# Performance work log

Measured on AMD Instinct MI355X. Metric: run time of the kernel, lower is better.

## Reference

```python
import jax, jax.numpy as jnp
import numpy as np

K = 1024   # codebook size
C = 8      # codebook channels
D = K // C # per-channel code dim = 128
BETA = 0.25
B = 8192   # batch of latent vectors, each of size C*D = K


def setup_inputs() -> dict:
    key = jax.random.key(0)
    k1, k2, k3 = jax.random.split(key, 3)
    latents = jax.random.normal(k1, (B, C * D), dtype=jnp.float32)
    # nn.Embedding(K, D) init: uniform(-1/K, 1/K)
    embedding = jax.random.uniform(k2, (K, D), dtype=jnp.float32,
                                   minval=-1.0 / K, maxval=1.0 / K)
    k = jax.random.randint(k3, (C,), 0, 8, dtype=jnp.int32)
    return {"latents": latents, "embedding": embedding, "k": k}


def reference(latents, embedding, k):
    sg = jax.lax.stop_gradient
    flat = latents.reshape(-1, D)                                  # [B*C, D]
    # squared euclidean distance to every code: [B*C, K]
    dist = (jnp.sum(flat ** 2, axis=1, keepdims=True)
            + jnp.sum(embedding ** 2, axis=1)
            - 2.0 * (flat @ embedding.T))
    order = jnp.argsort(dist, axis=1).reshape(-1, C, K)            # [B, C, K]
    # per channel c, pick the k[c]-th nearest code index
    sel = jnp.take_along_axis(order, k[None, :, None], axis=2)[..., 0]  # [B, C]
    # one-hot @ embedding == plain gather of selected rows
    quantized = embedding[sel.reshape(-1)].reshape(latents.shape)  # [B, C*D]
    commitment_loss = jnp.mean((sg(quantized) - latents) ** 2)
    embedding_loss = jnp.mean((quantized - sg(latents)) ** 2)
    vq_loss = BETA * commitment_loss + embedding_loss
    # straight-through estimator
    quantized_st = latents + sg(quantized - latents)
    return quantized_st, vq_loss
```

## Files before the change

kernel.cpp:

```cpp
#include <hip/hip_runtime.h>

#define KDIM   128
#define BM     64
#define NELEM  8388608

#define OFF_EBUF0 17408
#define OFF_ESQ   33792
#define OFF_FSQ   37888
#define OFF_SEL   38144
#define SMEM_SZ   38400

typedef __attribute__((ext_vector_type(8)))  short  short8;
typedef __attribute__((ext_vector_type(8)))  __bf16 bf16x8;
typedef __attribute__((ext_vector_type(4)))  float  f32x4;

__device__ inline ushort f2bf(float f) {
  unsigned u = __builtin_bit_cast(unsigned, f);
  u += 0x7fffu + ((u >> 16) & 1u);
  return (ushort)(u >> 16);
}
__device__ inline f32x4 mfma16(short8 a, short8 b, f32x4 c) {
  return __builtin_amdgcn_mfma_f32_16x16x32_bf16(
      __builtin_bit_cast(bf16x8, a), __builtin_bit_cast(bf16x8, b), c, 0, 0, 0);
}
__device__ inline void gload16(const void* g, void* l) {
  __builtin_amdgcn_global_load_lds(
      (const __attribute__((address_space(1))) unsigned*)g,
      (__attribute__((address_space(3))) unsigned*)l, 16, 0, 0);
}

__global__ void vq_prep(const float* __restrict__ emb, ushort* __restrict__ ebf,
                        float* __restrict__ esqm) {
  int j = blockIdx.x, d = threadIdx.x;
  float v = emb[j * KDIM + d];
  ebf[j * KDIM + (d ^ ((j & 7) << 3))] = f2bf(v);
  float s = v * v;
#pragma unroll
  for (int m = 1; m <= 32; m <<= 1) s += __shfl_xor(s, m);
  __shared__ float w[2];
  if ((threadIdx.x & 63) == 0) w[threadIdx.x >> 6] = s;
  __syncthreads();
  if (threadIdx.x == 0) esqm[j] = -0.5f * (w[0] + w[1]);
}

__global__ __launch_bounds__(256, 4) void vq_main(
    const float* __restrict__ lat, const float* __restrict__ emb,
    const int* __restrict__ ksel, const ushort* __restrict__ ebf,
    const float* __restrict__ esqm, float* __restrict__ out,
    float* __restrict__ partial) {
  __shared__ __align__(16) unsigned char smem[SMEM_SZ];
  ushort* fLds    = (ushort*)(smem);
  float*  esqmLds = (float*)(smem + OFF_ESQ);
  float*  fsqLds  = (float*)(smem + OFF_FSQ);
  int*    selLds  = (int*)(smem + OFF_SEL);

  const int tid = threadIdx.x;
  const int lane = tid & 63, wid = tid >> 6;
  const int gR0 = blockIdx.x * BM;

  {
    const char* src = (const char*)ebf + tid * 16;
    char* dst = (char*)smem + OFF_EBUF0 + tid * 16;
#pragma unroll
    for (int q = 0; q < 4; ++q) gload16(src + q * 4096, dst + q * 4096);
  }
  ((float4*)esqmLds)[tid] = ((const float4*)esqm)[tid];

#pragma unroll
  for (int it = 0; it < 8; ++it) {
    int i = tid + it * 256;
    int row = i >> 5, c4 = i & 31;
    float4 v = *(const float4*)(lat + (size_t)(gR0 + row) * KDIM + c4 * 4);
    float s = v.x * v.x + v.y * v.y + v.z * v.z + v.w * v.w;
#pragma unroll
    for (int m = 1; m <= 16; m <<= 1) s += __shfl_xor(s, m);
    if ((lane & 31) == 0) fsqLds[row] = s;
    ushort4 b; b.x = f2bf(v.x); b.y = f2bf(v.y); b.z = f2bf(v.z); b.w = f2bf(v.w);
    *(ushort4*)(&fLds[row * 136 + c4 * 4]) = b;
  }
  __syncthreads();

  const int n = lane & 15, hi = lane >> 4;
  short8 bfr[4];
  {
    const ushort* fp = &fLds[(wid * 16 + n) * 136 + hi * 8];
#pragma unroll
    for (int s = 0; s < 4; ++s) bfr[s] = *(const short8*)(fp + s * 32);
  }
  asm volatile("s_waitcnt lgkmcnt(0)" ::: "memory");

  const int nm = n & 7;
  const int pb = ((hi ^ (nm & 3)) << 4) | (((nm >> 2) & 1) << 6);
  const char* aE0 = (const char*)smem + OFF_EBUF0 + n * 256 + pb;
  const char* aO0 = (const char*)smem + OFF_EBUF0 + n * 256 + (pb ^ 64);
  const char* aE1 = (const char*)smem + 0 + n * 256 + pb;
  const char* aO1 = (const char*)smem + 0 + n * 256 + (pb ^ 64);

  int cst[4][4];
#pragma unroll
  for (int st = 0; st < 4; ++st)
#pragma unroll
    for (int r = 0; r < 4; ++r) cst[st][r] = st * 16 + hi * 4 + r;

  float top[8];
#pragma unroll
  for (int p = 0; p < 8; ++p) top[p] = __builtin_bit_cast(float, 0xFF800000u);

#pragma unroll 2
  for (int nn = 0; nn < 16; ++nn) {
    __builtin_amdgcn_s_barrier();
    if (nn < 15) {
      const char* src = (const char*)ebf + (nn + 1) * 16384 + tid * 16;
      char* dst = (char*)smem + ((nn & 1) ? OFF_EBUF0 : 0) + tid * 16;
#pragma unroll
      for (int q = 0; q < 4; ++q) gload16(src + q * 4096, dst + q * 4096);
      asm volatile("s_waitcnt vmcnt(4)" ::: "memory");
    } else {
      asm volatile("s_waitcnt vmcnt(0)" ::: "memory");
    }
    __builtin_amdgcn_s_barrier();

    const char* aEb = (nn & 1) ? aE1 : aE0;
    const char* aOb = (nn & 1) ? aO1 : aO0;

    f32x4 acc[4];
    {
      const float* eq = esqmLds + nn * 64 + hi * 4;
#pragma unroll
      for (int st = 0; st < 4; ++st) acc[st] = *(const f32x4*)(eq + st * 16);
    }

#pragma unroll
    for (int s = 0; s < 4; ++s) {
      const char* ab = (s & 1) ? aOb : aEb;
      const int so = (s >> 1) * 128;
#pragma unroll
      for (int st = 0; st < 4; ++st) {
        short8 a = *(const short8*)(ab + st * 4096 + so);
        acc[st] = mfma16(a, bfr[s], acc[st]);
      }
    }

#pragma unroll
    for (int cell = 0; cell < 2; ++cell) {
      float k[8];
#pragma unroll
      for (int st = 0; st < 2; ++st)
#pragma unroll
        for (int r = 0; r < 4; ++r) {
          unsigned bb = (__builtin_bit_cast(unsigned, acc[cell * 2 + st][r]) & 0xFFFFFC00u)
                        | (unsigned)cst[cell * 2 + st][r];
          k[st * 4 + r] = __builtin_bit_cast(float, bb);
        }
      float x = fmaxf(fmaxf(k[0], k[1]), k[2]);
      float y = fmaxf(fmaxf(k[3], k[4]), k[5]);
      float z = fmaxf(k[6], k[7]);
      float c = fmaxf(fmaxf(x, y), z);
      unsigned cb = __builtin_bit_cast(unsigned, c) | (unsigned)(nn << 6);
      float key = __builtin_bit_cast(float, cb);
#pragma unroll
      for (int p = 0; p < 8; ++p) {
        float mx = fmaxf(top[p], key);
        key = fminf(top[p], key);
        top[p] = mx;
      }
    }
  }

  float* mbuf = (float*)(smem + OFF_EBUF0);
  __syncthreads();
#pragma unroll
  for (int p = 0; p < 8; ++p) mbuf[p * 256 + tid] = top[p];
  __syncthreads();

  if (tid < 64) {
    const int b0 = (tid >> 4) * 64 + (tid & 15);
    int kk = ksel[tid & 7]; kk = kk < 0 ? 0 : (kk > 7 ? 7 : kk);
    float a0 = mbuf[b0], a1 = mbuf[b0 + 16], a2 = mbuf[b0 + 32], a3 = mbuf[b0 + 48];
    int i0 = 1, i1 = 1, i2 = 1, i3 = 1;
    float sel = a0;
    for (int s = 0; s <= kk; ++s) {
      float m01 = fmaxf(a0, a1), m23 = fmaxf(a2, a3);
      sel = fmaxf(m01, m23);
      if (sel == a0)      { a0 = mbuf[i0 * 256 + b0];      ++i0; }
      else if (sel == a1) { a1 = mbuf[i1 * 256 + b0 + 16]; ++i1; }
      else if (sel == a2) { a2 = mbuf[i2 * 256 + b0 + 32]; ++i2; }
      else                { a3 = mbuf[i3 * 256 + b0 + 48]; ++i3; }
    }
    unsigned sb = __builtin_bit_cast(unsigned, sel);
    selLds[tid] = (int)(sb & 1023u);
    float val = __builtin_bit_cast(float, sb & 0xFFFFFC00u);
    float rl = fsqLds[tid] - 2.0f * val;
#pragma unroll
    for (int m = 1; m <= 32; m <<= 1) rl += __shfl_xor(rl, m);
    if (tid == 0) partial[blockIdx.x] = rl;
  }
  __syncthreads();

#pragma unroll
  for (int it = 0; it < 8; ++it) {
    int i = tid + it * 256;
    int row = i >> 5, c4 = i & 31;
    int s2 = selLds[row];
    float4 q = *(const float4*)(emb + (size_t)s2 * KDIM + c4 * 4);
    *(float4*)(out + (size_t)(gR0 + row) * KDIM + c4 * 4) = q;
  }
}

__global__ void vq_reduce(const float* __restrict__ p, float* __restrict__ loss) {
  int t = threadIdx.x;
  double s = (double)p[t] + (double)p[t + 256] + (double)p[t + 512] + (double)p[t + 768];
#pragma unroll
  for (int m = 1; m <= 32; m <<= 1) s += __shfl_xor(s, m);
  __shared__ double w[4];
  if ((t & 63) == 0) w[t >> 6] = s;
  __syncthreads();
  if (t == 0) loss[0] = (float)((w[0] + w[1] + w[2] + w[3]) * (1.25 / 8388608.0));
}

extern "C" void kernel_launch(void* const* d_in, const int* in_sizes, int n_in,
                              void* d_out, int out_size, void* d_ws, size_t ws_size,
                              hipStream_t stream) {
  const float* lat = (const float*)d_in[0];
  const float* emb = (const float*)d_in[1];
  const int* ksel = (const int*)d_in[2];
  float* out = (float*)d_out;

  ushort* ebf = (ushort*)d_ws;
  float* esqm = (float*)((char*)d_ws + 262144);
  float* partial = (float*)((char*)d_ws + 266240);

  vq_prep<<<1024, 128, 0, stream>>>(emb, ebf, esqm);
  vq_main<<<1024, 256, 0, stream>>>(lat, emb, ksel, ebf, esqm, out, partial);
  vq_reduce<<<1, 256, 0, stream>>>(partial, out + NELEM);
}
```

Baseline: 44.49 us.

## Keep latent tiles in registers and stream codebook fragments directly from global

The main kernel no longer stages the bf16 codebook through double-buffered LDS with global-to-LDS loads. Instead each wave holds all 64 row fragments of its latent tile in registers and owns a quarter of the codebook (256 codes), loading A fragments straight from global/L2 with register double-buffering. Per-row top-8 lists are kept per wave-slice and merged across 16 sorted lists in a final 16-way selection, and the launch-bounds occupancy hint drops to 2 blocks. This removes LDS traffic and barriers in the inner loop, but raises register pressure and relies on L2 bandwidth for repeated codebook reads across all blocks.

```diff
diff --git a/kernel.cpp b/kernel.cpp
--- a/kernel.cpp
+++ b/kernel.cpp
@@ -3,12 +3,12 @@
 #define KDIM   128
 #define BM     64
 #define NELEM  8388608
-
-#define OFF_EBUF0 17408
-#define OFF_ESQ   33792
-#define OFF_FSQ   37888
-#define OFF_SEL   38144
-#define SMEM_SZ   38400
+#define FSTR   144
+
+#define OFF_ESQ 32768
+#define OFF_FSQ 36864
+#define OFF_SEL 37120
+#define SMEM_SZ 37376
 
 typedef __attribute__((ext_vector_type(8)))  short  short8;
 typedef __attribute__((ext_vector_type(8)))  __bf16 bf16x8;
@@ -23,17 +23,12 @@
   return __builtin_amdgcn_mfma_f32_16x16x32_bf16(
       __builtin_bit_cast(bf16x8, a), __builtin_bit_cast(bf16x8, b), c, 0, 0, 0);
 }
-__device__ inline void gload16(const void* g, void* l) {
-  __builtin_amdgcn_global_load_lds(
-      (const __attribute__((address_space(1))) unsigned*)g,
-      (__attribute__((address_space(3))) unsigned*)l, 16, 0, 0);
-}
 
 __global__ void vq_prep(const float* __restrict__ emb, ushort* __restrict__ ebf,
                         float* __restrict__ esqm) {
   int j = blockIdx.x, d = threadIdx.x;
   float v = emb[j * KDIM + d];
-  ebf[j * KDIM + (d ^ ((j & 7) << 3))] = f2bf(v);
+  ebf[j * KDIM + d] = f2bf(v);
   float s = v * v;
 #pragma unroll
   for (int m = 1; m <= 32; m <<= 1) s += __shfl_xor(s, m);
@@ -43,13 +38,14 @@
   if (threadIdx.x == 0) esqm[j] = -0.5f * (w[0] + w[1]);
 }
 
-__global__ __launch_bounds__(256, 4) void vq_main(
+__global__ __launch_bounds__(256, 2) void vq_main(
     const float* __restrict__ lat, const float* __restrict__ emb,
     const int* __restrict__ ksel, const ushort* __restrict__ ebf,
     const float* __restrict__ esqm, float* __restrict__ out,
     float* __restrict__ partial) {
   __shared__ __align__(16) unsigned char smem[SMEM_SZ];
   ushort* fLds    = (ushort*)(smem);
+  float*  mbuf    = (float*)(smem);
   float*  esqmLds = (float*)(smem + OFF_ESQ);
   float*  fsqLds  = (float*)(smem + OFF_FSQ);
   int*    selLds  = (int*)(smem + OFF_SEL);
@@ -58,12 +54,6 @@
   const int lane = tid & 63, wid = tid >> 6;
   const int gR0 = blockIdx.x * BM;
 
-  {
-    const char* src = (const char*)ebf + tid * 16;
-    char* dst = (char*)smem + OFF_EBUF0 + tid * 16;
-#pragma unroll
-    for (int q = 0; q < 4; ++q) gload16(src + q * 4096, dst + q * 4096);
-  }
   ((float4*)esqmLds)[tid] = ((const float4*)esqm)[tid];
 
 #pragma unroll
@@ -76,124 +66,121 @@
     for (int m = 1; m <= 16; m <<= 1) s += __shfl_xor(s, m);
     if ((lane & 31) == 0) fsqLds[row] = s;
     ushort4 b; b.x = f2bf(v.x); b.y = f2bf(v.y); b.z = f2bf(v.z); b.w = f2bf(v.w);
-    *(ushort4*)(&fLds[row * 136 + c4 * 4]) = b;
+    *(ushort4*)(&fLds[row * FSTR + c4 * 4]) = b;
   }
   __syncthreads();
 
   const int n = lane & 15, hi = lane >> 4;
-  short8 bfr[4];
-  {
-    const ushort* fp = &fLds[(wid * 16 + n) * 136 + hi * 8];
-#pragma unroll
-    for (int s = 0; s < 4; ++s) bfr[s] = *(const short8*)(fp + s * 32);
-  }
-  asm volatile("s_waitcnt lgkmcnt(0)" ::: "memory");
-
-  const int nm = n & 7;
-  const int pb = ((hi ^ (nm & 3)) << 4) | (((nm >> 2) & 1) << 6);
-  const char* aE0 = (const char*)smem + OFF_EBUF0 + n * 256 + pb;
-  const char* aO0 = (const char*)smem + OFF_EBUF0 + n * 256 + (pb ^ 64);
-  const char* aE1 = (const char*)smem + 0 + n * 256 + pb;
-  const char* aO1 = (const char*)smem + 0 + n * 256 + (pb ^ 64);
-
-  int cst[4][4];
-#pragma unroll
-  for (int st = 0; st < 4; ++st)
-#pragma unroll
-    for (int r = 0; r < 4; ++r) cst[st][r] = st * 16 + hi * 4 + r;
-
-  float top[8];
-#pragma unroll
-  for (int p = 0; p < 8; ++p) top[p] = __builtin_bit_cast(float, 0xFF800000u);
-
-#pragma unroll 2
-  for (int nn = 0; nn < 16; ++nn) {
-    __builtin_amdgcn_s_barrier();
-    if (nn < 15) {
-      const char* src = (const char*)ebf + (nn + 1) * 16384 + tid * 16;
-      char* dst = (char*)smem + ((nn & 1) ? OFF_EBUF0 : 0) + tid * 16;
-#pragma unroll
-      for (int q = 0; q < 4; ++q) gload16(src + q * 4096, dst + q * 4096);
-      asm volatile("s_waitcnt vmcnt(4)" ::: "memory");
-    } else {
-      asm volatile("s_waitcnt vmcnt(0)" ::: "memory");
-    }
-    __builtin_amdgcn_s_barrier();
-
-    const char* aEb = (nn & 1) ? aE1 : aE0;
-    const char* aOb = (nn & 1) ? aO1 : aO0;
-
-    f32x4 acc[4];
-    {
-      const float* eq = esqmLds + nn * 64 + hi * 4;
-#pragma unroll
-      for (int st = 0; st < 4; ++st) acc[st] = *(const f32x4*)(eq + st * 16);
-    }
-
-#pragma unroll
-    for (int s = 0; s < 4; ++s) {
-      const char* ab = (s & 1) ? aOb : aEb;
-      const int so = (s >> 1) * 128;
-#pragma unroll
-      for (int st = 0; st < 4; ++st) {
-        short8 a = *(const short8*)(ab + st * 4096 + so);
-        acc[st] = mfma16(a, bfr[s], acc[st]);
-      }
-    }
-
-#pragma unroll
-    for (int cell = 0; cell < 2; ++cell) {
+  short8 bfr[4][4];
+#pragma unroll
+  for (int ct = 0; ct < 4; ++ct)
+#pragma unroll
+    for (int s = 0; s < 4; ++s)
+      bfr[ct][s] = *(const short8*)(&fLds[(ct * 16 + n) * FSTR + s * 32 + hi * 8]);
+  __syncthreads();
+
+  const ushort* aBase = ebf + ((size_t)(wid * 256 + n) * KDIM) + hi * 8;
+
+  const float NINF = __builtin_bit_cast(float, 0xFF800000u);
+  float top[4][8];
+#pragma unroll
+  for (int ct = 0; ct < 4; ++ct)
+#pragma unroll
+    for (int p = 0; p < 8; ++p) top[ct][p] = NINF;
+
+  short8 afr[2][8];
+#pragma unroll
+  for (int u = 0; u < 2; ++u)
+#pragma unroll
+    for (int s = 0; s < 4; ++s)
+      afr[0][u * 4 + s] = *(const short8*)(aBase + u * 16 * KDIM + s * 32);
+
+#pragma unroll
+  for (int tp = 0; tp < 8; ++tp) {
+    if (tp < 7) {
+      const ushort* ap = aBase + (size_t)(tp + 1) * 32 * KDIM;
+#pragma unroll
+      for (int u = 0; u < 2; ++u)
+#pragma unroll
+        for (int s = 0; s < 4; ++s)
+          afr[(tp + 1) & 1][u * 4 + s] = *(const short8*)(ap + u * 16 * KDIM + s * 32);
+    }
+    f32x4 acc[2][4];
+#pragma unroll
+    for (int u = 0; u < 2; ++u) {
+      f32x4 e = *(const f32x4*)(esqmLds + wid * 256 + tp * 32 + u * 16 + hi * 4);
+#pragma unroll
+      for (int ct = 0; ct < 4; ++ct) acc[u][ct] = e;
+    }
+#pragma unroll
+    for (int s = 0; s < 4; ++s)
+#pragma unroll
+      for (int u = 0; u < 2; ++u)
+#pragma unroll
+        for (int ct = 0; ct < 4; ++ct)
+          acc[u][ct] = mfma16(afr[tp & 1][u * 4 + s], bfr[ct][s], acc[u][ct]);
+
+    const int cbase = wid * 256 + tp * 32 + hi * 4;
+#pragma unroll
+    for (int ct = 0; ct < 4; ++ct) {
       float k[8];
 #pragma unroll
-      for (int st = 0; st < 2; ++st)
+      for (int u = 0; u < 2; ++u)
 #pragma unroll
         for (int r = 0; r < 4; ++r) {
-          unsigned bb = (__builtin_bit_cast(unsigned, acc[cell * 2 + st][r]) & 0xFFFFFC00u)
-                        | (unsigned)cst[cell * 2 + st][r];
-          k[st * 4 + r] = __builtin_bit_cast(float, bb);
+          unsigned bb = (__builtin_bit_cast(unsigned, acc[u][ct][r]) & 0xFFFFFC00u)
+                        | (unsigned)(cbase + u * 16 + r);
+          k[u * 4 + r] = __builtin_bit_cast(float, bb);
         }
       float x = fmaxf(fmaxf(k[0], k[1]), k[2]);
       float y = fmaxf(fmaxf(k[3], k[4]), k[5]);
-      float z = fmaxf(k[6], k[7]);
-      float c = fmaxf(fmaxf(x, y), z);
-      unsigned cb = __builtin_bit_cast(unsigned, c) | (unsigned)(nn << 6);
-      float key = __builtin_bit_cast(float, cb);
+      float key = fmaxf(fmaxf(x, y), fmaxf(k[6], k[7]));
 #pragma unroll
       for (int p = 0; p < 8; ++p) {
-        float mx = fmaxf(top[p], key);
-        key = fminf(top[p], key);
-        top[p] = mx;
+        float mx = fmaxf(top[ct][p], key);
+        key = fminf(top[ct][p], key);
+        top[ct][p] = mx;
       }
     }
   }
 
-  float* mbuf = (float*)(smem + OFF_EBUF0);
-  __syncthreads();
-#pragma unroll
-  for (int p = 0; p < 8; ++p) mbuf[p * 256 + tid] = top[p];
+#pragma unroll
+  for (int ct = 0; ct < 4; ++ct) {
+    float* dst = mbuf + ((size_t)((ct * 16 + n) * 16 + ((wid * 4 + hi) ^ n))) * 8;
+    *(f32x4*)(dst + 0) = (f32x4){top[ct][0], top[ct][1], top[ct][2], top[ct][3]};
+    *(f32x4*)(dst + 4) = (f32x4){top[ct][4], top[ct][5], top[ct][6], top[ct][7]};
+  }
   __syncthreads();
 
   if (tid < 64) {
-    const int b0 = (tid >> 4) * 64 + (tid & 15);
-    int kk = ksel[tid & 7]; kk = kk < 0 ? 0 : (kk > 7 ? 7 : kk);
-    float a0 = mbuf[b0], a1 = mbuf[b0 + 16], a2 = mbuf[b0 + 32], a3 = mbuf[b0 + 48];
-    int i0 = 1, i1 = 1, i2 = 1, i3 = 1;
-    float sel = a0;
-    for (int s = 0; s <= kk; ++s) {
-      float m01 = fmaxf(a0, a1), m23 = fmaxf(a2, a3);
-      sel = fmaxf(m01, m23);
-      if (sel == a0)      { a0 = mbuf[i0 * 256 + b0];      ++i0; }
-      else if (sel == a1) { a1 = mbuf[i1 * 256 + b0 + 16]; ++i1; }
-      else if (sel == a2) { a2 = mbuf[i2 * 256 + b0 + 32]; ++i2; }
-      else                { a3 = mbuf[i3 * 256 + b0 + 48]; ++i3; }
+    const int L = tid, nx = L & 15;
+    int kk = ksel[L & 7]; kk = kk < 0 ? 0 : (kk > 7 ? 7 : kk);
+    float h[16]; int ix[16];
+#pragma unroll
+    for (int j = 0; j < 16; ++j) { h[j] = mbuf[(L * 16 + (j ^ nx)) * 8]; ix[j] = 0; }
+    float sel;
+    for (int s = 0;; ++s) {
+      float m01 = fmaxf(fmaxf(h[0], h[1]), fmaxf(h[2], h[3]));
+      float m23 = fmaxf(fmaxf(h[4], h[5]), fmaxf(h[6], h[7]));
+      float m45 = fmaxf(fmaxf(h[8], h[9]), fmaxf(h[10], h[11]));
+      float m67 = fmaxf(fmaxf(h[12], h[13]), fmaxf(h[14], h[15]));
+      sel = fmaxf(fmaxf(m01, m23), fmaxf(m45, m67));
+      if (s == kk) break;
+#pragma unroll
+      for (int j = 0; j < 16; ++j) {
+        if (h[j] == sel) {
+          ++ix[j];
+          h[j] = (ix[j] < 8) ? mbuf[(L * 16 + (j ^ nx)) * 8 + ix[j]] : NINF;
+        }
+      }
     }
     unsigned sb = __builtin_bit_cast(unsigned, sel);
-    selLds[tid] = (int)(sb & 1023u);
+    selLds[L] = (int)(sb & 1023u);
     float val = __builtin_bit_cast(float, sb & 0xFFFFFC00u);
-    float rl = fsqLds[tid] - 2.0f * val;
+    float rl = fsqLds[L] - 2.0f * val;
 #pragma unroll
     for (int m = 1; m <= 32; m <<= 1) rl += __shfl_xor(rl, m);
-    if (tid == 0) partial[blockIdx.x] = rl;
+    if (L == 0) partial[blockIdx.x] = rl;
   }
   __syncthreads();
 
```

After: 62.61 us. 1.41x slower.
